# Performance work log

Measured on AMD Instinct MI355X. Metric: run time of the kernel, lower is better.

The kernel has to match this reference:

```python
import jax, jax.numpy as jnp
import numpy as np
from jax.ops import segment_sum

N = 100000


def _gcn_conv(h, W, b, row, col, dinv_row_col):
    # h: [N, d_in] -> [N, d_out]; PyG GCNConv: x@W, symmetric-normalized scatter-add, +bias
    h = h @ W
    msg = h[row] * dinv_row_col[:, None]          # [E+N, d_out]
    out = segment_sum(msg, col, num_segments=N)   # scatter-add to destination nodes
    return out + b


def setup_inputs() -> dict:
    key = jax.random.key(0)
    k1, k2, k3, k4, k5, k6 = jax.random.split(key, 6)
    E = 1200000
    x = jax.random.normal(k1, (N, 128), dtype=jnp.float32)
    edge_index = jax.random.randint(k2, (2, E), 0, N, dtype=jnp.int64)
    W1 = jax.random.normal(k3, (128, 64), dtype=jnp.float32) * (1.0 / np.sqrt(128))
    b1 = jax.random.normal(k4, (64,), dtype=jnp.float32) * 0.02
    W2 = jax.random.normal(k5, (64, 40), dtype=jnp.float32) * (1.0 / np.sqrt(64))
    b2 = jax.random.normal(k6, (40,), dtype=jnp.float32) * 0.02
    return {"x": x, "edge_index": edge_index, "W1": W1, "b1": b1, "W2": W2, "b2": b2}


def reference(x, edge_index, W1, b1, W2, b2):
    # Add self-loops (PyG GCNConv default add_self_loops=True)
    loop = jnp.arange(N, dtype=edge_index.dtype)
    row = jnp.concatenate([edge_index[0], loop])  # source
    col = jnp.concatenate([edge_index[1], loop])  # destination
    # Symmetric normalization: deg from destination (incl. self loops)
    deg = segment_sum(jnp.ones_like(col, dtype=x.dtype), col, num_segments=N)
    dinv = jnp.where(deg > 0, jax.lax.rsqrt(deg), 0.0)
    dinv_rc = dinv[row] * dinv[col]               # [E+N]

    hid = _gcn_conv(x, W1, b1, row, col, dinv_rc)
    hid = jax.nn.leaky_relu(hid, negative_slope=0.01)
    # dropout p=0 -> identity
    out = _gcn_conv(hid, W2, b2, row, col, dinv_rc)
    return out
```

## Files before the change

### kernel.cpp

```cpp
#include <hip/hip_runtime.h>

#define NN 100000
#define EE 1200000
#define NB 391
#define EPB 4096
#define BIN_BLK 293

typedef _Float16 half4 __attribute__((ext_vector_type(4)));

__global__ __launch_bounds__(256) void k_zero_b(int* __restrict__ bcnt) {
  int i = blockIdx.x * 256 + threadIdx.x;
  if (i < NB) bcnt[i] = 0;
}

__global__ __launch_bounds__(256) void k_binhist(const int* __restrict__ col, int* __restrict__ bcnt) {
  __shared__ int lh[NB];
  int t = threadIdx.x;
  for (int i = t; i < NB; i += 256) lh[i] = 0;
  __syncthreads();
  int base = blockIdx.x * EPB;
  #pragma unroll
  for (int i = 0; i < 16; ++i) {
    int e = base + i * 256 + t;
    if (e < EE) atomicAdd(&lh[col[e] >> 8], 1);
  }
  __syncthreads();
  for (int i = t; i < NB; i += 256) {
    int v = lh[i];
    if (v) atomicAdd(&bcnt[i], v);
  }
}

__global__ __launch_bounds__(512) void k_binscan(const int* __restrict__ bcnt, int* __restrict__ bptr,
                                                 int* __restrict__ bcur, int* __restrict__ row_ptr) {
  __shared__ int sm[512];
  int t = threadIdx.x;
  int v = (t < NB) ? bcnt[t] : 0;
  sm[t] = v;
  __syncthreads();
  for (int off = 1; off < 512; off <<= 1) {
    int u = (t >= off) ? sm[t - off] : 0;
    __syncthreads();
    sm[t] += u;
    __syncthreads();
  }
  int excl = sm[t] - v;
  if (t < NB) { bptr[t] = excl; bcur[t] = excl; }
  if (t == 0) { bptr[NB] = EE; row_ptr[NN] = EE; }
}

__global__ __launch_bounds__(256) void k_binfill(const int* __restrict__ row, const int* __restrict__ col,
                                                 int* __restrict__ bcur, int* __restrict__ binned) {
  __shared__ int lh[NB];
  __shared__ int lbase[NB];
  int t = threadIdx.x;
  for (int i = t; i < NB; i += 256) lh[i] = 0;
  __syncthreads();
  int base = blockIdx.x * EPB;
  #pragma unroll
  for (int i = 0; i < 16; ++i) {
    int e = base + i * 256 + t;
    if (e < EE) atomicAdd(&lh[col[e] >> 8], 1);
  }
  __syncthreads();
  for (int i = t; i < NB; i += 256) {
    int v = lh[i];
    lbase[i] = v ? atomicAdd(&bcur[i], v) : 0;
  }
  __syncthreads();
  for (int i = t; i < NB; i += 256) lh[i] = 0;
  __syncthreads();
  #pragma unroll
  for (int i = 0; i < 16; ++i) {
    int e = base + i * 256 + t;
    if (e < EE) {
      int c = col[e];
      int b = c >> 8;
      int p = lbase[b] + atomicAdd(&lh[b], 1);
      binned[p] = (row[e] << 8) | (c & 255);
    }
  }
}

__global__ __launch_bounds__(256) void k_build2(const int* __restrict__ binned, const int* __restrict__ bptr,
                                                int* __restrict__ row_ptr, int* __restrict__ src,
                                                float* __restrict__ dinv) {
  __shared__ int cnt[256];
  __shared__ int sm[256];
  __shared__ int cur[256];
  int t = threadIdx.x;
  int b = blockIdx.x;
  int nb0 = b << 8;
  int nnode = NN - nb0 < 256 ? NN - nb0 : 256;
  int ebeg = bptr[b], eend = bptr[b + 1];
  cnt[t] = 0;
  __syncthreads();
  for (int e = ebeg + t; e < eend; e += 256)
    atomicAdd(&cnt[binned[e] & 255], 1);
  __syncthreads();
  int v = cnt[t];
  sm[t] = v;
  __syncthreads();
  for (int off = 1; off < 256; off <<= 1) {
    int u = (t >= off) ? sm[t - off] : 0;
    __syncthreads();
    sm[t] += u;
    __syncthreads();
  }
  int excl = sm[t] - v;
  if (t < nnode) {
    row_ptr[nb0 + t] = ebeg + excl;
    dinv[nb0 + t] = rsqrtf((float)v + 1.0f);
  }
  cur[t] = excl;
  __syncthreads();
  for (int e = ebeg + t; e < eend; e += 256) {
    int rc = binned[e];
    int cl = rc & 255;
    int p = ebeg + atomicAdd(&cur[cl], 1);
    src[p] = rc >> 8;
  }
}

__global__ __launch_bounds__(256) void k_gemm1(const float* __restrict__ x, const float* __restrict__ W,
                                               const float* __restrict__ dinv, _Float16* __restrict__ g) {
  __shared__ __align__(16) float Ws[128 * 64];
  __shared__ __align__(16) float xs[64][68];
  const int t = threadIdx.x;
  const int row0 = blockIdx.x * 64;

  #pragma unroll
  for (int p = 0; p < 8; ++p) {
    int i = (t + p * 256) * 4;
    *reinterpret_cast<float4*>(&Ws[i]) = *reinterpret_cast<const float4*>(&W[i]);
  }

  const int rq = t >> 4;
  const int cq = t & 15;
  float a[4][4];
  #pragma unroll
  for (int i = 0; i < 4; ++i)
    #pragma unroll
    for (int j = 0; j < 4; ++j) a[i][j] = 0.0f;

  for (int kc = 0; kc < 2; ++kc) {
    __syncthreads();
    #pragma unroll
    for (int p = 0; p < 4; ++p) {
      int idx = t + p * 256;
      int r = idx >> 4;
      int k4 = (idx & 15) << 2;
      int grow = row0 + r;
      float4 v = make_float4(0.f, 0.f, 0.f, 0.f);
      if (grow < NN) v = *reinterpret_cast<const float4*>(&x[(size_t)grow * 128 + kc * 64 + k4]);
      xs[k4 + 0][r] = v.x;
      xs[k4 + 1][r] = v.y;
      xs[k4 + 2][r] = v.z;
      xs[k4 + 3][r] = v.w;
    }
    __syncthreads();
    #pragma unroll 8
    for (int k = 0; k < 64; ++k) {
      float4 xv = *reinterpret_cast<const float4*>(&xs[k][rq * 4]);
      float4 wv = *reinterpret_cast<const float4*>(&Ws[(kc * 64 + k) * 64 + cq * 4]);
      a[0][0] = fmaf(xv.x, wv.x, a[0][0]); a[0][1] = fmaf(xv.x, wv.y, a[0][1]);
      a[0][2] = fmaf(xv.x, wv.z, a[0][2]); a[0][3] = fmaf(xv.x, wv.w, a[0][3]);
      a[1][0] = fmaf(xv.y, wv.x, a[1][0]); a[1][1] = fmaf(xv.y, wv.y, a[1][1]);
      a[1][2] = fmaf(xv.y, wv.z, a[1][2]); a[1][3] = fmaf(xv.y, wv.w, a[1][3]);
      a[2][0] = fmaf(xv.z, wv.x, a[2][0]); a[2][1] = fmaf(xv.z, wv.y, a[2][1]);
      a[2][2] = fmaf(xv.z, wv.z, a[2][2]); a[2][3] = fmaf(xv.z, wv.w, a[2][3]);
      a[3][0] = fmaf(xv.w, wv.x, a[3][0]); a[3][1] = fmaf(xv.w, wv.y, a[3][1]);
      a[3][2] = fmaf(xv.w, wv.z, a[3][2]); a[3][3] = fmaf(xv.w, wv.w, a[3][3]);
    }
  }
  #pragma unroll
  for (int i = 0; i < 4; ++i) {
    int grow = row0 + rq * 4 + i;
    if (grow < NN) {
      float dv = dinv[grow];
      half4 h;
      h.x = (_Float16)(a[i][0] * dv);
      h.y = (_Float16)(a[i][1] * dv);
      h.z = (_Float16)(a[i][2] * dv);
      h.w = (_Float16)(a[i][3] * dv);
      *reinterpret_cast<half4*>(&g[(size_t)grow * 64 + cq * 4]) = h;
    }
  }
}

__global__ __launch_bounds__(256) void k_gather1(const int* __restrict__ row_ptr, const int* __restrict__ src,
                                                 const _Float16* __restrict__ g, const float* __restrict__ dinv,
                                                 const float* __restrict__ b1, float* __restrict__ hid) {
  int t = threadIdx.x;
  int node = blockIdx.x * 16 + (t >> 4);
  if (node >= NN) return;
  int q = (t & 15) << 2;
  int beg = row_ptr[node], end = row_ptr[node + 1];
  half4 sv = *reinterpret_cast<const half4*>(&g[(size_t)node * 64 + q]);
  float4 acc = make_float4((float)sv.x, (float)sv.y, (float)sv.z, (float)sv.w);
  int e = beg;
  for (; e + 3 < end; e += 4) {
    int s0 = src[e], s1 = src[e + 1], s2 = src[e + 2], s3 = src[e + 3];
    half4 v0 = *reinterpret_cast<const half4*>(&g[(size_t)s0 * 64 + q]);
    half4 v1 = *reinterpret_cast<const half4*>(&g[(size_t)s1 * 64 + q]);
    half4 v2 = *reinterpret_cast<const half4*>(&g[(size_t)s2 * 64 + q]);
    half4 v3 = *reinterpret_cast<const half4*>(&g[(size_t)s3 * 64 + q]);
    acc.x += ((float)v0.x + (float)v1.x) + ((float)v2.x + (float)v3.x);
    acc.y += ((float)v0.y + (float)v1.y) + ((float)v2.y + (float)v3.y);
    acc.z += ((float)v0.z + (float)v1.z) + ((float)v2.z + (float)v3.z);
    acc.w += ((float)v0.w + (float)v1.w) + ((float)v2.w + (float)v3.w);
  }
  for (; e < end; ++e) {
    int s0 = src[e];
    half4 v0 = *reinterpret_cast<const half4*>(&g[(size_t)s0 * 64 + q]);
    acc.x += (float)v0.x; acc.y += (float)v0.y; acc.z += (float)v0.z; acc.w += (float)v0.w;
  }
  float dv = dinv[node];
  float4 bv = *reinterpret_cast<const float4*>(&b1[q]);
  float4 o;
  o.x = acc.x * dv + bv.x; o.y = acc.y * dv + bv.y;
  o.z = acc.z * dv + bv.z; o.w = acc.w * dv + bv.w;
  o.x = o.x > 0.f ? o.x : 0.01f * o.x;
  o.y = o.y > 0.f ? o.y : 0.01f * o.y;
  o.z = o.z > 0.f ? o.z : 0.01f * o.z;
  o.w = o.w > 0.f ? o.w : 0.01f * o.w;
  *reinterpret_cast<float4*>(&hid[(size_t)node * 64 + q]) = o;
}

__global__ __launch_bounds__(256) void k_gemm2(const float* __restrict__ hid, const float* __restrict__ W,
                                               const float* __restrict__ dinv, _Float16* __restrict__ g2) {
  __shared__ __align__(16) float Ws[64 * 40];
  __shared__ __align__(16) float xs[64][132];
  const int t = threadIdx.x;
  const int row0 = blockIdx.x * 128;

  for (int i = t; i < 640; i += 256)
    *reinterpret_cast<float4*>(&Ws[i * 4]) = *reinterpret_cast<const float4*>(&W[i * 4]);

  #pragma unroll
  for (int p = 0; p < 8; ++p) {
    int idx = t + p * 256;
    int r = idx >> 4;
    int k4 = (idx & 15) << 2;
    int grow = row0 + r;
    float4 v = make_float4(0.f, 0.f, 0.f, 0.f);
    if (grow < NN) v = *reinterpret_cast<const float4*>(&hid[(size_t)grow * 64 + k4]);
    xs[k4 + 0][r] = v.x;
    xs[k4 + 1][r] = v.y;
    xs[k4 + 2][r] = v.z;
    xs[k4 + 3][r] = v.w;
  }
  __syncthreads();

  const int rq = t >> 3;
  const int cq = t & 7;
  float a[4][5];
  #pragma unroll
  for (int i = 0; i < 4; ++i)
    #pragma unroll
    for (int j = 0; j < 5; ++j) a[i][j] = 0.0f;

  #pragma unroll 8
  for (int k = 0; k < 64; ++k) {
    float4 xv = *reinterpret_cast<const float4*>(&xs[k][rq * 4]);
    float w0 = Ws[k * 40 + cq * 5 + 0];
    float w1 = Ws[k * 40 + cq * 5 + 1];
    float w2 = Ws[k * 40 + cq * 5 + 2];
    float w3 = Ws[k * 40 + cq * 5 + 3];
    float w4 = Ws[k * 40 + cq * 5 + 4];
    a[0][0] = fmaf(xv.x, w0, a[0][0]); a[0][1] = fmaf(xv.x, w1, a[0][1]);
    a[0][2] = fmaf(xv.x, w2, a[0][2]); a[0][3] = fmaf(xv.x, w3, a[0][3]);
    a[0][4] = fmaf(xv.x, w4, a[0][4]);
    a[1][0] = fmaf(xv.y, w0, a[1][0]); a[1][1] = fmaf(xv.y, w1, a[1][1]);
    a[1][2] = fmaf(xv.y, w2, a[1][2]); a[1][3] = fmaf(xv.y, w3, a[1][3]);
    a[1][4] = fmaf(xv.y, w4, a[1][4]);
    a[2][0] = fmaf(xv.z, w0, a[2][0]); a[2][1] = fmaf(xv.z, w1, a[2][1]);
    a[2][2] = fmaf(xv.z, w2, a[2][2]); a[2][3] = fmaf(xv.z, w3, a[2][3]);
    a[2][4] = fmaf(xv.z, w4, a[2][4]);
    a[3][0] = fmaf(xv.w, w0, a[3][0]); a[3][1] = fmaf(xv.w, w1, a[3][1]);
    a[3][2] = fmaf(xv.w, w2, a[3][2]); a[3][3] = fmaf(xv.w, w3, a[3][3]);
    a[3][4] = fmaf(xv.w, w4, a[3][4]);
  }

  #pragma unroll
  for (int i = 0; i < 4; ++i) {
    int grow = row0 + rq * 4 + i;
    if (grow < NN) {
      float dv = dinv[grow];
      #pragma unroll
      for (int j = 0; j < 5; ++j)
        g2[(size_t)grow * 40 + cq * 5 + j] = (_Float16)(a[i][j] * dv);
    }
  }
}

__global__ __launch_bounds__(320) void k_gather2(const int* __restrict__ row_ptr, const int* __restrict__ src,
                                                 const _Float16* __restrict__ g2, const float* __restrict__ dinv,
                                                 const float* __restrict__ b2, float* __restrict__ out) {
  int t = threadIdx.x;
  int local = t / 10;
  int grp = t - local * 10;
  int node = blockIdx.x * 32 + local;
  if (node >= NN) return;
  int q = grp * 4;
  int beg = row_ptr[node], end = row_ptr[node + 1];
  half4 sv = *reinterpret_cast<const half4*>(&g2[(size_t)node * 40 + q]);
  float4 acc = make_float4((float)sv.x, (float)sv.y, (float)sv.z, (float)sv.w);
  int e = beg;
  for (; e + 3 < end; e += 4) {
    int s0 = src[e], s1 = src[e + 1], s2 = src[e + 2], s3 = src[e + 3];
    half4 v0 = *reinterpret_cast<const half4*>(&g2[(size_t)s0 * 40 + q]);
    half4 v1 = *reinterpret_cast<const half4*>(&g2[(size_t)s1 * 40 + q]);
    half4 v2 = *reinterpret_cast<const half4*>(&g2[(size_t)s2 * 40 + q]);
    half4 v3 = *reinterpret_cast<const half4*>(&g2[(size_t)s3 * 40 + q]);
    acc.x += ((float)v0.x + (float)v1.x) + ((float)v2.x + (float)v3.x);
    acc.y += ((float)v0.y + (float)v1.y) + ((float)v2.y + (float)v3.y);
    acc.z += ((float)v0.z + (float)v1.z) + ((float)v2.z + (float)v3.z);
    acc.w += ((float)v0.w + (float)v1.w) + ((float)v2.w + (float)v3.w);
  }
  for (; e < end; ++e) {
    int s0 = src[e];
    half4 v0 = *reinterpret_cast<const half4*>(&g2[(size_t)s0 * 40 + q]);
    acc.x += (float)v0.x; acc.y += (float)v0.y; acc.z += (float)v0.z; acc.w += (float)v0.w;
  }
  float dv = dinv[node];
  float4 bv = *reinterpret_cast<const float4*>(&b2[q]);
  float4 o;
  o.x = acc.x * dv + bv.x; o.y = acc.y * dv + bv.y;
  o.z = acc.z * dv + bv.z; o.w = acc.w * dv + bv.w;
  *reinterpret_cast<float4*>(&out[(size_t)node * 40 + q]) = o;
}

extern "C" void kernel_launch(void* const* d_in, const int* in_sizes, int n_in,
                              void* d_out, int out_size, void* d_ws, size_t ws_size,
                              hipStream_t stream) {
  const float* x  = (const float*)d_in[0];
  const int*   ei = (const int*)d_in[1];
  const float* W1 = (const float*)d_in[2];
  const float* b1 = (const float*)d_in[3];
  const float* W2 = (const float*)d_in[4];
  const float* b2 = (const float*)d_in[5];
  float* out = (float*)d_out;

  const int* row = ei;
  const int* col = ei + EE;

  float* ws      = (float*)d_ws;
  float* dinv    = ws;
  int*   row_ptr = (int*)(ws + 100352);
  int*   bptr    = row_ptr + 100352;
  int*   bcnt    = bptr + 512;
  int*   bcur    = bcnt + 512;
  int*   src     = bcur + 512;
  _Float16* g1   = (_Float16*)(src + 1200128);
  float* hid     = (float*)((char*)g1 + 12800000);
  _Float16* g2   = g1;
  int*   binned  = (int*)g1;

  k_zero_b <<<2, 256, 0, stream>>>(bcnt);
  k_binhist<<<BIN_BLK, 256, 0, stream>>>(col, bcnt);
  k_binscan<<<1, 512, 0, stream>>>(bcnt, bptr, bcur, row_ptr);
  k_binfill<<<BIN_BLK, 256, 0, stream>>>(row, col, bcur, binned);
  k_build2 <<<NB, 256, 0, stream>>>(binned, bptr, row_ptr, src, dinv);

  k_gemm1  <<<(NN + 63) / 64, 256, 0, stream>>>(x, W1, dinv, g1);
  k_gather1<<<(NN + 15) / 16, 256, 0, stream>>>(row_ptr, src, g1, dinv, b1, hid);

  k_gemm2  <<<(NN + 127) / 128, 256, 0, stream>>>(hid, W2, dinv, g2);
  k_gather2<<<(NN + 31) / 32, 320, 0, stream>>>(row_ptr, src, g2, dinv, b2, out);
}
```

Measured before the change: 245.7 us.

## Use fp16 MFMA for both GCN linear layers and store hidden activations in fp16

Both dense projection kernels now use the matrix-core 16x16x32 fp16 MFMA instruction in place of scalar FP32 FMA loops. Inputs and weights are converted to fp16 in shared memory, with the weights stored transposed. The hidden activation buffer written by the first gather is now fp16, which halves its write and read traffic. The trade is reduced precision in the inputs and weights, plus narrow scalar fp16 stores of the outputs.

```diff
diff --git a/kernel.cpp b/kernel.cpp
--- a/kernel.cpp
+++ b/kernel.cpp
@@ -7,6 +7,8 @@
 #define BIN_BLK 293
 
 typedef _Float16 half4 __attribute__((ext_vector_type(4)));
+typedef _Float16 half8 __attribute__((ext_vector_type(8)));
+typedef float    f32x4 __attribute__((ext_vector_type(4)));
 
 __global__ __launch_bounds__(256) void k_zero_b(int* __restrict__ bcnt) {
   int i = blockIdx.x * 256 + threadIdx.x;
@@ -124,73 +126,78 @@
 
 __global__ __launch_bounds__(256) void k_gemm1(const float* __restrict__ x, const float* __restrict__ W,
                                                const float* __restrict__ dinv, _Float16* __restrict__ g) {
-  __shared__ __align__(16) float Ws[128 * 64];
-  __shared__ __align__(16) float xs[64][68];
+  __shared__ _Float16 xh[64 * 136];
+  __shared__ _Float16 Wt[64 * 136];
   const int t = threadIdx.x;
   const int row0 = blockIdx.x * 64;
 
   #pragma unroll
   for (int p = 0; p < 8; ++p) {
-    int i = (t + p * 256) * 4;
-    *reinterpret_cast<float4*>(&Ws[i]) = *reinterpret_cast<const float4*>(&W[i]);
-  }
-
-  const int rq = t >> 4;
-  const int cq = t & 15;
-  float a[4][4];
-  #pragma unroll
-  for (int i = 0; i < 4; ++i)
+    int idx = t + p * 256;
+    int k = idx >> 4;
+    int n4 = (idx & 15) << 2;
+    float4 v = *reinterpret_cast<const float4*>(&W[k * 64 + n4]);
+    Wt[(n4 + 0) * 136 + k] = (_Float16)v.x;
+    Wt[(n4 + 1) * 136 + k] = (_Float16)v.y;
+    Wt[(n4 + 2) * 136 + k] = (_Float16)v.z;
+    Wt[(n4 + 3) * 136 + k] = (_Float16)v.w;
+  }
+  #pragma unroll
+  for (int p = 0; p < 4; ++p) {
+    int idx = t + p * 256;
+    int r = idx >> 4;
+    int k8 = idx & 15;
+    int grow = row0 + r;
+    half8 h = {0, 0, 0, 0, 0, 0, 0, 0};
+    if (grow < NN) {
+      float4 a0 = *reinterpret_cast<const float4*>(&x[(size_t)grow * 128 + k8 * 8]);
+      float4 a1 = *reinterpret_cast<const float4*>(&x[(size_t)grow * 128 + k8 * 8 + 4]);
+      h[0] = (_Float16)a0.x; h[1] = (_Float16)a0.y; h[2] = (_Float16)a0.z; h[3] = (_Float16)a0.w;
+      h[4] = (_Float16)a1.x; h[5] = (_Float16)a1.y; h[6] = (_Float16)a1.z; h[7] = (_Float16)a1.w;
+    }
+    *reinterpret_cast<half8*>(&xh[r * 136 + k8 * 8]) = h;
+  }
+  __syncthreads();
+
+  const int w = t >> 6;
+  const int l = t & 63;
+  const int lrow = l & 15;
+  const int kg = l >> 4;
+
+  f32x4 z = {0.0f, 0.0f, 0.0f, 0.0f};
+  f32x4 acc[4];
+  acc[0] = z; acc[1] = z; acc[2] = z; acc[3] = z;
+
+  const _Float16* xb = &xh[(w * 16 + lrow) * 136 + kg * 8];
+  #pragma unroll
+  for (int s = 0; s < 4; ++s) {
+    half8 a = *reinterpret_cast<const half8*>(xb + s * 32);
     #pragma unroll
-    for (int j = 0; j < 4; ++j) a[i][j] = 0.0f;
-
-  for (int kc = 0; kc < 2; ++kc) {
-    __syncthreads();
+    for (int nt = 0; nt < 4; ++nt) {
+      half8 b = *reinterpret_cast<const half8*>(&Wt[(nt * 16 + lrow) * 136 + kg * 8 + s * 32]);
+      acc[nt] = __builtin_amdgcn_mfma_f32_16x16x32_f16(a, b, acc[nt], 0, 0, 0);
+    }
+  }
+
+  float dv[4];
+  #pragma unroll
+  for (int r = 0; r < 4; ++r) {
+    int grow = row0 + w * 16 + kg * 4 + r;
+    dv[r] = (grow < NN) ? dinv[grow] : 0.0f;
+  }
+  #pragma unroll
+  for (int nt = 0; nt < 4; ++nt)
     #pragma unroll
-    for (int p = 0; p < 4; ++p) {
-      int idx = t + p * 256;
-      int r = idx >> 4;
-      int k4 = (idx & 15) << 2;
-      int grow = row0 + r;
-      float4 v = make_float4(0.f, 0.f, 0.f, 0.f);
-      if (grow < NN) v = *reinterpret_cast<const float4*>(&x[(size_t)grow * 128 + kc * 64 + k4]);
-      xs[k4 + 0][r] = v.x;
-      xs[k4 + 1][r] = v.y;
-      xs[k4 + 2][r] = v.z;
-      xs[k4 + 3][r] = v.w;
-    }
-    __syncthreads();
-    #pragma unroll 8
-    for (int k = 0; k < 64; ++k) {
-      float4 xv = *reinterpret_cast<const float4*>(&xs[k][rq * 4]);
-      float4 wv = *reinterpret_cast<const float4*>(&Ws[(kc * 64 + k) * 64 + cq * 4]);
-      a[0][0] = fmaf(xv.x, wv.x, a[0][0]); a[0][1] = fmaf(xv.x, wv.y, a[0][1]);
-      a[0][2] = fmaf(xv.x, wv.z, a[0][2]); a[0][3] = fmaf(xv.x, wv.w, a[0][3]);
-      a[1][0] = fmaf(xv.y, wv.x, a[1][0]); a[1][1] = fmaf(xv.y, wv.y, a[1][1]);
-      a[1][2] = fmaf(xv.y, wv.z, a[1][2]); a[1][3] = fmaf(xv.y, wv.w, a[1][3]);
-      a[2][0] = fmaf(xv.z, wv.x, a[2][0]); a[2][1] = fmaf(xv.z, wv.y, a[2][1]);
-      a[2][2] = fmaf(xv.z, wv.z, a[2][2]); a[2][3] = fmaf(xv.z, wv.w, a[2][3]);
-      a[3][0] = fmaf(xv.w, wv.x, a[3][0]); a[3][1] = fmaf(xv.w, wv.y, a[3][1]);
-      a[3][2] = fmaf(xv.w, wv.z, a[3][2]); a[3][3] = fmaf(xv.w, wv.w, a[3][3]);
-    }
-  }
-  #pragma unroll
-  for (int i = 0; i < 4; ++i) {
-    int grow = row0 + rq * 4 + i;
-    if (grow < NN) {
-      float dv = dinv[grow];
-      half4 h;
-      h.x = (_Float16)(a[i][0] * dv);
-      h.y = (_Float16)(a[i][1] * dv);
-      h.z = (_Float16)(a[i][2] * dv);
-      h.w = (_Float16)(a[i][3] * dv);
-      *reinterpret_cast<half4*>(&g[(size_t)grow * 64 + cq * 4]) = h;
-    }
-  }
+    for (int r = 0; r < 4; ++r) {
+      int grow = row0 + w * 16 + kg * 4 + r;
+      if (grow < NN)
+        g[(size_t)grow * 64 + nt * 16 + lrow] = (_Float16)(acc[nt][r] * dv[r]);
+    }
 }
 
 __global__ __launch_bounds__(256) void k_gather1(const int* __restrict__ row_ptr, const int* __restrict__ src,
                                                  const _Float16* __restrict__ g, const float* __restrict__ dinv,
-                                                 const float* __restrict__ b1, float* __restrict__ hid) {
+                                                 const float* __restrict__ b1, _Float16* __restrict__ hid) {
   int t = threadIdx.x;
   int node = blockIdx.x * 16 + (t >> 4);
   if (node >= NN) return;
@@ -224,72 +231,71 @@
   o.y = o.y > 0.f ? o.y : 0.01f * o.y;
   o.z = o.z > 0.f ? o.z : 0.01f * o.z;
   o.w = o.w > 0.f ? o.w : 0.01f * o.w;
-  *reinterpret_cast<float4*>(&hid[(size_t)node * 64 + q]) = o;
-}
-
-__global__ __launch_bounds__(256) void k_gemm2(const float* __restrict__ hid, const float* __restrict__ W,
+  half4 ho;
+  ho.x = (_Float16)o.x; ho.y = (_Float16)o.y; ho.z = (_Float16)o.z; ho.w = (_Float16)o.w;
+  *reinterpret_cast<half4*>(&hid[(size_t)node * 64 + q]) = ho;
+}
+
+__global__ __launch_bounds__(256) void k_gemm2(const _Float16* __restrict__ hid, const float* __restrict__ W,
                                                const float* __restrict__ dinv, _Float16* __restrict__ g2) {
-  __shared__ __align__(16) float Ws[64 * 40];
-  __shared__ __align__(16) float xs[64][132];
+  __shared__ _Float16 xh[64 * 72];
+  __shared__ _Float16 Wt[48 * 72];
   const int t = threadIdx.x;
-  const int row0 = blockIdx.x * 128;
-
-  for (int i = t; i < 640; i += 256)
-    *reinterpret_cast<float4*>(&Ws[i * 4]) = *reinterpret_cast<const float4*>(&W[i * 4]);
-
-  #pragma unroll
-  for (int p = 0; p < 8; ++p) {
+  const int row0 = blockIdx.x * 64;
+
+  #pragma unroll
+  for (int p = 0; p < 12; ++p) {
     int idx = t + p * 256;
-    int r = idx >> 4;
-    int k4 = (idx & 15) << 2;
+    int n = idx >> 6, k = idx & 63;
+    _Float16 v = (_Float16)0.0f;
+    if (n < 40) v = (_Float16)W[k * 40 + n];
+    Wt[n * 72 + k] = v;
+  }
+  #pragma unroll
+  for (int p = 0; p < 2; ++p) {
+    int idx = t + p * 256;
+    int r = idx >> 3, k8 = idx & 7;
     int grow = row0 + r;
-    float4 v = make_float4(0.f, 0.f, 0.f, 0.f);
-    if (grow < NN) v = *reinterpret_cast<const float4*>(&hid[(size_t)grow * 64 + k4]);
-    xs[k4 + 0][r] = v.x;
-    xs[k4 + 1][r] = v.y;
-    xs[k4 + 2][r] = v.z;
-    xs[k4 + 3][r] = v.w;
-  }
-  __syncthreads();
-
-  const int rq = t >> 3;
-  const int cq = t & 7;
-  float a[4][5];
-  #pragma unroll
-  for (int i = 0; i < 4; ++i)
+    half8 h = {0, 0, 0, 0, 0, 0, 0, 0};
+    if (grow < NN) h = *reinterpret_cast<const half8*>(&hid[(size_t)grow * 64 + k8 * 8]);
+    *reinterpret_cast<half8*>(&xh[r * 72 + k8 * 8]) = h;
+  }
+  __syncthreads();
+
+  const int w = t >> 6;
+  const int l = t & 63;
+  const int lrow = l & 15;
+  const int kg = l >> 4;
+
+  f32x4 z = {0.0f, 0.0f, 0.0f, 0.0f};
+  f32x4 acc[3];
+  acc[0] = z; acc[1] = z; acc[2] = z;
+
+  const _Float16* xb = &xh[(w * 16 + lrow) * 72 + kg * 8];
+  #pragma unroll
+  for (int s = 0; s < 2; ++s) {
+    half8 a = *reinterpret_cast<const half8*>(xb + s * 32);
     #pragma unroll
-    for (int j = 0; j < 5; ++j) a[i][j] = 0.0f;
-
-  #pragma unroll 8
-  for (int k = 0; k < 64; ++k) {
-    float4 xv = *reinterpret_cast<const float4*>(&xs[k][rq * 4]);
-    float w0 = Ws[k * 40 + cq * 5 + 0];
-    float w1 = Ws[k * 40 + cq * 5 + 1];
-    float w2 = Ws[k * 40 + cq * 5 + 2];
-    float w3 = Ws[k * 40 + cq * 5 + 3];
-    float w4 = Ws[k * 40 + cq * 5 + 4];
-    a[0][0] = fmaf(xv.x, w0, a[0][0]); a[0][1] = fmaf(xv.x, w1, a[0][1]);
-    a[0][2] = fmaf(xv.x, w2, a[0][2]); a[0][3] = fmaf(xv.x, w3, a[0][3]);
-    a[0][4] = fmaf(xv.x, w4, a[0][4]);
-    a[1][0] = fmaf(xv.y, w0, a[1][0]); a[1][1] = fmaf(xv.y, w1, a[1][1]);
-    a[1][2] = fmaf(xv.y, w2, a[1][2]); a[1][3] = fmaf(xv.y, w3, a[1][3]);
-    a[1][4] = fmaf(xv.y, w4, a[1][4]);
-    a[2][0] = fmaf(xv.z, w0, a[2][0]); a[2][1] = fmaf(xv.z, w1, a[2][1]);
-    a[2][2] = fmaf(xv.z, w2, a[2][2]); a[2][3] = fmaf(xv.z, w3, a[2][3]);
-    a[2][4] = fmaf(xv.z, w4, a[2][4]);
-    a[3][0] = fmaf(xv.w, w0, a[3][0]); a[3][1] = fmaf(xv.w, w1, a[3][1]);
-    a[3][2] = fmaf(xv.w, w2, a[3][2]); a[3][3] = fmaf(xv.w, w3, a[3][3]);
-    a[3][4] = fmaf(xv.w, w4, a[3][4]);
-  }
-
-  #pragma unroll
-  for (int i = 0; i < 4; ++i) {
-    int grow = row0 + rq * 4 + i;
-    if (grow < NN) {
-      float dv = dinv[grow];
-      #pragma unroll
-      for (int j = 0; j < 5; ++j)
-        g2[(size_t)grow * 40 + cq * 5 + j] = (_Float16)(a[i][j] * dv);
+    for (int nt = 0; nt < 3; ++nt) {
+      half8 b = *reinterpret_cast<const half8*>(&Wt[(nt * 16 + lrow) * 72 + kg * 8 + s * 32]);
+      acc[nt] = __builtin_amdgcn_mfma_f32_16x16x32_f16(a, b, acc[nt], 0, 0, 0);
+    }
+  }
+
+  float dv[4];
+  #pragma unroll
+  for (int r = 0; r < 4; ++r) {
+    int grow = row0 + w * 16 + kg * 4 + r;
+    dv[r] = (grow < NN) ? dinv[grow] : 0.0f;
+  }
+  #pragma unroll
+  for (int nt = 0; nt < 3; ++nt) {
+    int colv = nt * 16 + lrow;
+    #pragma unroll
+    for (int r = 0; r < 4; ++r) {
+      int grow = row0 + w * 16 + kg * 4 + r;
+      if (grow < NN && colv < 40)
+        g2[(size_t)grow * 40 + colv] = (_Float16)(acc[nt][r] * dv[r]);
     }
   }
 }
@@ -353,7 +359,7 @@
   int*   bcur    = bcnt + 512;
   int*   src     = bcur + 512;
   _Float16* g1   = (_Float16*)(src + 1200128);
-  float* hid     = (float*)((char*)g1 + 12800000);
+  _Float16* hid  = (_Float16*)((char*)g1 + 12800000);
   _Float16* g2   = g1;
   int*   binned  = (int*)g1;
 
@@ -366,6 +372,6 @@
   k_gemm1  <<<(NN + 63) / 64, 256, 0, stream>>>(x, W1, dinv, g1);
   k_gather1<<<(NN + 15) / 16, 256, 0, stream>>>(row_ptr, src, g1, dinv, b1, hid);
 
-  k_gemm2  <<<(NN + 127) / 128, 256, 0, stream>>>(hid, W2, dinv, g2);
+  k_gemm2  <<<(NN + 63) / 64, 256, 0, stream>>>(hid, W2, dinv, g2);
   k_gather2<<<(NN + 31) / 32, 320, 0, stream>>>(row_ptr, src, g2, dinv, b2, out);
 }
```

New measurement: 228.3 us. 7.1% less time.
